# Kernel tuning notes

Measured on AMD Instinct MI355X. Metric: run time of the kernel, lower is better.

The kernel has to match this reference:

```python
import jax, jax.numpy as jnp
import numpy as np

N_HEAD = 16
D_HEAD = 64
D_LATENT = 32
BLOCK_SIZE = 2048


def rope_cache(dim, max_seq_len, theta=10000.0):
    inv_freq = 1.0 / (theta ** (jnp.arange(0, dim, 2, dtype=jnp.float32) / dim))
    t = jnp.arange(max_seq_len, dtype=jnp.float32)
    freqs = jnp.einsum('i,j->ij', t, inv_freq)        # [T, dim/2]
    emb = jnp.concatenate([freqs, freqs], axis=-1)    # [T, dim]
    return jnp.cos(emb), jnp.sin(emb)


def apply_rope(x, cos, sin):
    # x: [B, H, T, C]; interleaved-pair rotation as in the torch module
    B, H, T, C = x.shape
    c = cos[:T][None, None]
    s = sin[:T][None, None]
    x1 = x[..., 0::2]
    x2 = x[..., 1::2]
    rotated = jnp.stack((-x2, x1), axis=-1).reshape(B, H, T, C)
    return x * c + rotated * s


def setup_inputs() -> dict:
    key = jax.random.key(0)
    ks = jax.random.split(key, 7)
    sd = 0.02
    return {
        'x':   jax.random.normal(ks[0], (2, 2048, 1024), dtype=jnp.float32),
        'Wq':  jax.random.normal(ks[1], (1024, 1024), dtype=jnp.float32) * sd,
        'Wk':  jax.random.normal(ks[2], (512, 1024), dtype=jnp.float32) * sd,
        'Wv':  jax.random.normal(ks[3], (512, 1024), dtype=jnp.float32) * sd,
        'Wku': jax.random.normal(ks[4], (64, 32), dtype=jnp.float32) * sd,
        'Wvu': jax.random.normal(ks[5], (64, 32), dtype=jnp.float32) * sd,
        'Wc':  jax.random.normal(ks[6], (1024, 1024), dtype=jnp.float32) * sd,
    }


def reference(x, Wq, Wk, Wv, Wku, Wvu, Wc):
    B, T, C = x.shape
    H, Dh, Dl = N_HEAD, D_HEAD, D_LATENT

    # latent KV (compressed cache entries)
    k_lat = (x @ Wk.T).reshape(B, T, H, Dl)   # [B,T,H,Dl]
    v_lat = (x @ Wv.T).reshape(B, T, H, Dl)

    # q and up-projected k/v -> [B,H,T,Dh]
    q = (x @ Wq.T).reshape(B, T, H, Dh).transpose(0, 2, 1, 3)
    k = jnp.einsum('bthl,dl->bhtd', k_lat, Wku)
    v = jnp.einsum('bthl,dl->bhtd', v_lat, Wvu)

    cos, sin = rope_cache(Dh, BLOCK_SIZE)
    q = apply_rope(q, cos, sin)
    k = apply_rope(k, cos, sin)

    scale = 1.0 / jnp.sqrt(jnp.asarray(Dh, dtype=x.dtype))
    att = jnp.einsum('bhqd,bhkd->bhqk', q, k) * scale   # [B,H,T,T]
    causal = jnp.tril(jnp.ones((T, T), dtype=bool))
    att = jnp.where(causal[None, None], att, -jnp.inf)
    att = jax.nn.softmax(att, axis=-1)

    y = jnp.einsum('bhqk,bhkd->bhqd', att, v)           # [B,H,T,Dh]
    y = y.transpose(0, 2, 1, 3).reshape(B, T, C) @ Wc.T  # [B,T,C]
    return y, k_lat, v_lat
```

## Files before the change

### kernel.cpp

```cpp
#include <hip/hip_runtime.h>
#include <math.h>

#define NHEAD  16
#define DHEAD  64
#define DLAT   32
#define TSEQ   2048
#define NBATCH 2
#define CDIM   1024
#define MROWS  (NBATCH*TSEQ)

typedef __attribute__((ext_vector_type(8))) short bf16x8;
typedef __attribute__((ext_vector_type(4))) short bf16x4;
typedef __attribute__((ext_vector_type(4))) float f32x4;

#define AS1 __attribute__((address_space(1)))
#define AS3 __attribute__((address_space(3)))

__device__ __forceinline__ unsigned short f2bf(float f) {
    union { float f; unsigned u; } v; v.f = f;
    unsigned r = v.u + 0x7fff + ((v.u >> 16) & 1);
    return (unsigned short)(r >> 16);
}

__device__ __forceinline__ unsigned pk2(float lo, float hi) {
    return (unsigned)f2bf(lo) | ((unsigned)f2bf(hi) << 16);
}

__device__ __forceinline__ unsigned pack_trunc(float hi, float lo) {
    return __builtin_amdgcn_perm(__float_as_uint(hi), __float_as_uint(lo), 0x07060302u);
}

__device__ __forceinline__ void gld_lds16(const unsigned short* g, unsigned short* l) {
    __builtin_amdgcn_global_load_lds((const AS1 void*)g, (AS3 void*)l, 16, 0, 0);
}

__device__ __forceinline__ f32x4 mfma_16x16x16_bf16(bf16x4 a, bf16x4 b, f32x4 c) {
#if __has_builtin(__builtin_amdgcn_mfma_f32_16x16x16bf16_1k)
    return __builtin_amdgcn_mfma_f32_16x16x16bf16_1k(a, b, c, 0, 0, 0);
#else
    asm volatile("v_mfma_f32_16x16x16_bf16 %0, %1, %2, %0\n\ts_nop 4"
                 : "+v"(c) : "v"(a), "v"(b));
    return c;
#endif
}

#define QSCALE 0.18033688011112042f
#define RFREQ  0.28782313662425572f

__global__ __launch_bounds__(256) void cvt_all(
        const float* __restrict__ x,  const float* __restrict__ wq,
        const float* __restrict__ wk, const float* __restrict__ wv,
        const float* __restrict__ wc, const float* __restrict__ wku,
        const float* __restrict__ wvu,
        unsigned short* __restrict__ xb, unsigned short* __restrict__ wall) {
    int i = (blockIdx.x * 256 + threadIdx.x) * 4;
    const float* src; unsigned short* dst; int off;
    if      (i < 4194304) { src = x;   dst = xb;             off = 0;       }
    else if (i < 5242880) { src = wq;  dst = wall;           off = 4194304; }
    else if (i < 5767168) { src = wk;  dst = wall + 1048576; off = 5242880; }
    else if (i < 6291456) { src = wv;  dst = wall + 1572864; off = 5767168; }
    else if (i < 7340032) { src = wc;  dst = wall + 2097152; off = 6291456; }
    else if (i < 7342080) { src = wku; dst = wall + 3145728; off = 7340032; }
    else                  { src = wvu; dst = wall + 3147776; off = 7342080; }
    float4 v = *(const float4*)(src + (i - off));
    ushort4 o = { f2bf(v.x), f2bf(v.y), f2bf(v.z), f2bf(v.w) };
    *(ushort4*)(dst + (i - off)) = o;
}

__device__ __forceinline__ void gemm_core(
        const unsigned short* __restrict__ A, const unsigned short* __restrict__ W,
        int K, int bm, int bn, unsigned short* As, unsigned short* Bs,
        f32x4 (&acc)[2][2]) {
    const int tid = threadIdx.x;
    const int w = tid >> 6, lane = tid & 63;
    const int quad = lane >> 4, l16 = lane & 15;
    const int wm = (w >> 1) * 32, wn = (w & 1) * 32;

    const int r8 = lane >> 3, c8 = lane & 7;
    const int scl = (c8 ^ r8) * 8;

    const unsigned short* Ag0 = A + (size_t)(bm +      w*8 + r8) * K + scl;
    const unsigned short* Ag1 = A + (size_t)(bm + 64 + w*8 + r8) * K + scl;
    const unsigned short* Wg0 = W + (size_t)(bn +      w*8 + r8) * K + scl;
    unsigned short* AsD0 = &As[(     w*8) * 64];
    unsigned short* AsD1 = &As[(64 + w*8) * 64];
    unsigned short* BsD  = &Bs[(     w*8) * 64];

    const int fx0 = (quad ^ (l16 & 7)) * 8;
    const int fx1 = ((quad + 4) ^ (l16 & 7)) * 8;

    for (int k0 = 0; k0 < K; k0 += 64) {
        gld_lds16(Ag0 + k0, AsD0);
        gld_lds16(Ag1 + k0, AsD1);
        gld_lds16(Wg0 + k0, BsD);
        __syncthreads();
        bf16x8 af0[2], af1[2], bf0[2], bf1[2];
        #pragma unroll
        for (int t = 0; t < 2; ++t) {
            af0[t] = *(const bf16x8*)&As[(wm + t*16 + l16)*64 + fx0];
            af1[t] = *(const bf16x8*)&As[(wm + t*16 + l16)*64 + fx1];
        }
        #pragma unroll
        for (int c = 0; c < 2; ++c) {
            bf0[c] = *(const bf16x8*)&Bs[(wn + c*16 + l16)*64 + fx0];
            bf1[c] = *(const bf16x8*)&Bs[(wn + c*16 + l16)*64 + fx1];
        }
        #pragma unroll
        for (int t = 0; t < 2; ++t)
            #pragma unroll
            for (int c = 0; c < 2; ++c) {
                acc[t][c] = __builtin_amdgcn_mfma_f32_16x16x32_bf16(af0[t], bf0[c], acc[t][c], 0, 0, 0);
                acc[t][c] = __builtin_amdgcn_mfma_f32_16x16x32_bf16(af1[t], bf1[c], acc[t][c], 0, 0, 0);
            }
        __syncthreads();
    }
}

__global__ __launch_bounds__(512, 4) void gemm_proj(
        const unsigned short* __restrict__ A, const unsigned short* __restrict__ W,
        unsigned short* __restrict__ qbo, float* __restrict__ okl,
        float* __restrict__ ovl, int K) {
    __shared__ unsigned short As[128*64];
    __shared__ unsigned short Bs[64*64];
    const int bm = blockIdx.y * 128, bn = blockIdx.x * 64;
    f32x4 acc[2][2] = {};
    gemm_core(A, W, K, bm, bn, As, Bs, acc);

    const int tid = threadIdx.x;
    const int w = tid >> 6, lane = tid & 63;
    const int quad = lane >> 4, l16 = lane & 15;
    const int wm = (w >> 1) * 32, wn = (w & 1) * 32;

    if (bn < 1024) {
        const int h = bn >> 6;
        const int p = l16 & 1;
        const float invf0 = __expf(-(float)(l16)      * RFREQ);
        const float invf1 = __expf(-(float)(16 + l16) * RFREQ);
        #pragma unroll
        for (int t = 0; t < 2; ++t)
            #pragma unroll
            for (int r = 0; r < 4; ++r) {
                int row = bm + wm + t*16 + quad*4 + r;
                int ts  = row & 2047;
                float tf = (float)ts;
                size_t obase = (((size_t)((row >> 11)*16 + h))*TSEQ + ts)*DHEAD;
                #pragma unroll
                for (int c = 0; c < 2; ++c) {
                    float x  = acc[t][c][r];
                    float px = __shfl_xor(x, 1, 64);
                    float sv, cv;
                    __sincosf(tf * (c ? invf1 : invf0), &sv, &cv);
                    float o = (x*cv + (p ? px : -px)*sv) * QSCALE;
                    float po = __shfl_xor(o, 1, 64);
                    if (!p) {
                        unsigned pr = pk2(o, po);
                        *(unsigned*)&qbo[obase + wn + c*16 + l16] = pr;
                    }
                }
            }
    } else {
        float* base; int ldo;
        if (bn < 1536) { base = okl + (bn - 1024); ldo = 512; }
        else           { base = ovl + (bn - 1536); ldo = 512; }
        #pragma unroll
        for (int t = 0; t < 2; ++t)
            #pragma unroll
            for (int c = 0; c < 2; ++c)
                #pragma unroll
                for (int r = 0; r < 4; ++r) {
                    int row = bm + wm + t*16 + quad*4 + r;
                    int col = wn + c*16 + l16;
                    base[(size_t)row * ldo + col] = acc[t][c][r];
                }
    }
}

__global__ __launch_bounds__(512, 4) void gemm_out(
        const unsigned short* __restrict__ A, const unsigned short* __restrict__ W,
        float* __restrict__ O, int N, int K) {
    __shared__ unsigned short As[128*64];
    __shared__ unsigned short Bs[64*64];
    const int bm = blockIdx.y * 128, bn = blockIdx.x * 64;
    f32x4 acc[2][2] = {};
    gemm_core(A, W, K, bm, bn, As, Bs, acc);

    const int tid = threadIdx.x;
    const int w = tid >> 6, lane = tid & 63;
    const int quad = lane >> 4, l16 = lane & 15;
    const int wm = (w >> 1) * 32, wn = (w & 1) * 32;
    #pragma unroll
    for (int t = 0; t < 2; ++t)
        #pragma unroll
        for (int c = 0; c < 2; ++c)
            #pragma unroll
            for (int r = 0; r < 4; ++r) {
                int row = bm + wm + t*16 + quad*4 + r;
                int col = bn + wn + c*16 + l16;
                O[(size_t)row * N + col] = acc[t][c][r];
            }
}

__global__ __launch_bounds__(256) void latup(
        const float* __restrict__ klat, const float* __restrict__ vlat,
        const unsigned short* __restrict__ wkub, const unsigned short* __restrict__ wvub,
        unsigned short* __restrict__ kb, unsigned short* __restrict__ vt) {
    __shared__ __attribute__((aligned(16))) unsigned short ksh[4][16][72];
    __shared__ __attribute__((aligned(16))) unsigned short vsh[4][64][24];

    const int bh = blockIdx.y, b = bh >> 4, h = bh & 15;
    const int tid = threadIdx.x, w = tid >> 6, lane = tid & 63;
    const int quad = lane >> 4, l16 = lane & 15;
    const int tw = blockIdx.x * 64 + w * 16;
    const int t  = tw + l16;

    const float* klp = klat + ((size_t)(b*TSEQ + t))*(NHEAD*DLAT) + h*DLAT + quad*8;
    const float* vlp = vlat + ((size_t)(b*TSEQ + t))*(NHEAD*DLAT) + h*DLAT + quad*8;
    float4 kA = *(const float4*)klp, kB = *(const float4*)(klp + 4);
    float4 vA = *(const float4*)vlp, vB = *(const float4*)(vlp + 4);

    bf16x8 xk[4], xv[4];
    #pragma unroll
    for (int c = 0; c < 4; ++c) {
        xk[c] = *(const bf16x8*)&wkub[(c*16 + l16)*DLAT + quad*8];
        xv[c] = *(const bf16x8*)&wvub[(c*16 + l16)*DLAT + quad*8];
    }

    union { bf16x8 v; unsigned u[4]; } yk, yv;
    yk.u[0] = pk2(kA.x, kA.y); yk.u[1] = pk2(kA.z, kA.w);
    yk.u[2] = pk2(kB.x, kB.y); yk.u[3] = pk2(kB.z, kB.w);
    yv.u[0] = pk2(vA.x, vA.y); yv.u[1] = pk2(vA.z, vA.w);
    yv.u[2] = pk2(vB.x, vB.y); yv.u[3] = pk2(vB.z, vB.w);

    f32x4 aK[4], aV[4];
    #pragma unroll
    for (int c = 0; c < 4; ++c) {
        f32x4 z = {0.f, 0.f, 0.f, 0.f};
        aK[c] = __builtin_amdgcn_mfma_f32_16x16x32_bf16(xk[c], yk.v, z, 0, 0, 0);
        aV[c] = __builtin_amdgcn_mfma_f32_16x16x32_bf16(xv[c], yv.v, z, 0, 0, 0);
    }

    float C0[4], S0[4], C1[4], S1[4];
    const float tf = (float)t;
    #pragma unroll
    for (int j = 0; j < 4; ++j) {
        float f0 = (float)(quad*4 + j);
        __sincosf(tf * __expf(-f0 * RFREQ),          &S0[j], &C0[j]);
        __sincosf(tf * __expf(-(f0 + 16.f) * RFREQ), &S1[j], &C1[j]);
    }

    #pragma unroll
    for (int c = 0; c < 4; ++c) {
        const float* Cs = (c & 1) ? C1 : C0;
        const float* Ss = (c & 1) ? S1 : S0;
        float a0 = aK[c][0], a1 = aK[c][1], a2 = aK[c][2], a3 = aK[c][3];
        unsigned kw0 = pk2(a0*Cs[0] - a1*Ss[0], a1*Cs[1] + a0*Ss[1]);
        unsigned kw1 = pk2(a2*Cs[2] - a3*Ss[2], a3*Cs[3] + a2*Ss[3]);
        *(uint2*)&ksh[w][l16][c*16 + quad*4] = make_uint2(kw0, kw1);

        vsh[w][c*16 + quad*4 + 0][l16] = f2bf(aV[c][0]);
        vsh[w][c*16 + quad*4 + 1][l16] = f2bf(aV[c][1]);
        vsh[w][c*16 + quad*4 + 2][l16] = f2bf(aV[c][2]);
        vsh[w][c*16 + quad*4 + 3][l16] = f2bf(aV[c][3]);
    }

    __asm__ __volatile__("s_waitcnt lgkmcnt(0)" ::: "memory");

    const int ro = lane >> 2, co = (lane & 3) * 16;
    size_t go = ((size_t)bh*TSEQ + tw + ro)*DHEAD + co;
    int4 k0o = *(const int4*)&ksh[w][ro][co];
    int4 k1o = *(const int4*)&ksh[w][ro][co + 8];
    *(int4*)&kb[go]     = k0o;
    *(int4*)&kb[go + 8] = k1o;

    size_t vo = ((size_t)bh*DHEAD + lane)*TSEQ + tw;
    int4 v0o = *(const int4*)&vsh[w][lane][0];
    int4 v1o = *(const int4*)&vsh[w][lane][8];
    *(int4*)&vt[vo]     = v0o;
    *(int4*)&vt[vo + 8] = v1o;
}

__device__ __forceinline__ void online_sm(f32x4 (&s)[8], float& m_run, float& l_run,
                                          f32x4 (&o)[4]) {
    float mx = -1e30f;
    #pragma unroll
    for (int c = 0; c < 8; ++c)
        #pragma unroll
        for (int r = 0; r < 4; ++r) mx = fmaxf(mx, s[c][r]);
    mx = fmaxf(mx, __shfl_xor(mx, 16, 64));
    mx = fmaxf(mx, __shfl_xor(mx, 32, 64));
    if (!__all(mx <= m_run + 8.f)) {
        float mn = fmaxf(m_run, mx);
        float alpha = __builtin_exp2f(m_run - mn);
        m_run = mn;
        l_run *= alpha;
        #pragma unroll
        for (int c = 0; c < 4; ++c)
            #pragma unroll
            for (int r = 0; r < 4; ++r) o[c][r] *= alpha;
    }
    float ls = 0.f;
    #pragma unroll
    for (int c = 0; c < 8; ++c)
        #pragma unroll
        for (int r = 0; r < 4; ++r) {
            float p = __builtin_exp2f(s[c][r] - m_run);
            s[c][r] = p;
            ls += p;
        }
    ls += __shfl_xor(ls, 16, 64);
    ls += __shfl_xor(ls, 32, 64);
    l_run += ls;
}

__global__ __launch_bounds__(512, 4) void flash_attn(
        const unsigned short* __restrict__ qb, const unsigned short* __restrict__ kb,
        const unsigned short* __restrict__ vtb, unsigned short* __restrict__ yatt) {
    const int bh = blockIdx.x;
    const int b = bh >> 4, h = bh & 15;

    __shared__ unsigned short Ks[2][128][64];
    __shared__ unsigned short VTs[2][64][128];

    const int tid  = threadIdx.x;
    const int w    = tid >> 6;
    const int lane = tid & 63;
    const int quad = lane >> 4;
    const int l16  = lane & 15;
    const bool heavy = (w >= 4);
    const int wq = w & 3;

    const int qtA = blockIdx.y;
    const int qtB = 31 - qtA;
    const int qt  = heavy ? qtB : qtA;
    const int myN = (qt + 2) >> 1;
    const int nB  = (qtB + 2) >> 1;

    const unsigned short* Kbase = kb  + (size_t)bh * TSEQ * DHEAD;
    const unsigned short* Vbase = vtb + (size_t)bh * DHEAD * TSEQ;

    const int kr8 = lane >> 3, kc8 = lane & 7;
    const int kcl = (kc8 ^ kr8) * 8;
    const int vr4 = lane >> 4, vcp = lane & 15;

    const int kx0 = (quad ^ (l16 & 7)) * 8;
    const int kx1 = ((quad + 4) ^ (l16 & 7)) * 8;
    const int vq = (quad >> 1), vodd = (quad & 1) * 4;

    const unsigned short* qbase =
        qb + ((size_t)bh*TSEQ + qt*64 + wq*16 + l16) * DHEAD + quad*8;
    bf16x8 q0 = *(const bf16x8*)qbase;
    bf16x8 q1 = *(const bf16x8*)(qbase + 32);

    f32x4 oacc[4] = {};
    float m_run = -1e30f, l_run = 0.f;

    #pragma unroll
    for (int i = 0; i < 2; ++i) {
        gld_lds16(Kbase + (size_t)(w*16 + i*8 + kr8)*DHEAD + kcl,
                  &Ks[0][w*16 + i*8][0]);
        int vrow = w*8 + i*4 + vr4;
        int vcl = (vcp ^ (vrow & 15)) * 8;
        gld_lds16(Vbase + (size_t)vrow*TSEQ + vcl, &VTs[0][w*8 + i*4][0]);
    }
    __syncthreads();

    for (int j = 0; j < nB; ++j) {
        const int buf = j & 1;
        if (j + 1 < nB) {
            const int kc = (j + 1) * 128;
            #pragma unroll
            for (int i = 0; i < 2; ++i) {
                gld_lds16(Kbase + (size_t)(kc + w*16 + i*8 + kr8)*DHEAD + kcl,
                          &Ks[buf^1][w*16 + i*8][0]);
                int vrow = w*8 + i*4 + vr4;
                int vcl = (vcp ^ (vrow & 15)) * 8;
                gld_lds16(Vbase + (size_t)vrow*TSEQ + kc + vcl,
                          &VTs[buf^1][w*8 + i*4][0]);
            }
        }

        if (j < myN) {
            f32x4 s[8];
            __builtin_amdgcn_s_setprio(1);
            #pragma unroll
            for (int c = 0; c < 8; ++c) {
                bf16x8 ak0 = *(const bf16x8*)&Ks[buf][c*16 + l16][kx0];
                bf16x8 ak1 = *(const bf16x8*)&Ks[buf][c*16 + l16][kx1];
                f32x4 z = {0.f, 0.f, 0.f, 0.f};
                z = __builtin_amdgcn_mfma_f32_16x16x32_bf16(ak0, q0, z, 0, 0, 0);
                z = __builtin_amdgcn_mfma_f32_16x16x32_bf16(ak1, q1, z, 0, 0, 0);
                s[c] = z;
            }
            __builtin_amdgcn_s_setprio(0);

            if (j == myN - 1) {
                #pragma unroll
                for (int c = 0; c < 8; ++c)
                    #pragma unroll
                    for (int r = 0; r < 4; ++r)
                        if (j*128 + c*16 + quad*4 + r > qt*64 + wq*16 + l16)
                            s[c][r] = -1e30f;
            }

            online_sm(s, m_run, l_run, oacc);

            __builtin_amdgcn_s_setprio(1);
            #pragma unroll
            for (int c = 0; c < 8; ++c) {
                union { bf16x4 v; unsigned u[2]; } bP;
                bP.u[0] = pack_trunc(s[c][1], s[c][0]);
                bP.u[1] = pack_trunc(s[c][3], s[c][2]);
                const int vcol = ((2*c + vq) ^ l16) * 8 + vodd;
                #pragma unroll
                for (int dc = 0; dc < 4; ++dc) {
                    bf16x4 av = *(const bf16x4*)&VTs[buf][dc*16 + l16][vcol];
                    oacc[dc] = mfma_16x16x16_bf16(av, bP.v, oacc[dc]);
                }
            }
            __builtin_amdgcn_s_setprio(0);
        }

        __syncthreads();
    }

    float invl = 1.0f / l_run;
    unsigned short* Wt = &Ks[0][0][0] + w * (16*72);
    #pragma unroll
    for (int c = 0; c < 4; ++c)
        #pragma unroll
        for (int r = 0; r < 4; ++r)
            Wt[(size_t)l16*72 + c*16 + quad*4 + r] = f2bf(oacc[c][r] * invl);
    __asm__ __volatile__("" ::: "memory");
    #pragma unroll
    for (int p = 0; p < 2; ++p) {
        int row = p*8 + (lane >> 3);
        int d0 = (lane & 7) * 8;
        int4 val = *(const int4*)&Wt[row*72 + d0];
        int tg = qt*64 + wq*16 + row;
        *(int4*)&yatt[((size_t)(b*TSEQ + tg))*CDIM + h*DHEAD + d0] = val;
    }
}

extern "C" void kernel_launch(void* const* d_in, const int* in_sizes, int n_in,
                              void* d_out, int out_size, void* d_ws, size_t ws_size,
                              hipStream_t stream) {
    const float* x   = (const float*)d_in[0];
    const float* Wq  = (const float*)d_in[1];
    const float* Wk  = (const float*)d_in[2];
    const float* Wv  = (const float*)d_in[3];
    const float* Wku = (const float*)d_in[4];
    const float* Wvu = (const float*)d_in[5];
    const float* Wc  = (const float*)d_in[6];

    float* out_y  = (float*)d_out;
    float* out_kl = out_y  + (size_t)MROWS * CDIM;
    float* out_vl = out_kl + (size_t)MROWS * NHEAD*DLAT;

    float* qproj = (float*)d_ws;
    unsigned short* xb   = (unsigned short*)(qproj + (size_t)MROWS*CDIM);
    unsigned short* qb   = xb  + (size_t)MROWS*CDIM;
    unsigned short* kb   = qb  + (size_t)MROWS*CDIM;
    unsigned short* vt   = kb  + (size_t)MROWS*CDIM;
    unsigned short* wall = vt  + (size_t)MROWS*CDIM;
    unsigned short* wcb  = wall + (size_t)2048*CDIM;
    unsigned short* wkub = wall + 3145728;
    unsigned short* wvub = wall + 3147776;
    unsigned short* yatt = (unsigned short*)qproj;

    cvt_all<<<7172, 256, 0, stream>>>(x, Wq, Wk, Wv, Wc, Wku, Wvu, xb, wall);

    gemm_proj<<<dim3(2048/64, MROWS/128), 512, 0, stream>>>(
        xb, wall, qb, out_kl, out_vl, CDIM);

    latup<<<dim3(TSEQ/64, NBATCH*NHEAD), 256, 0, stream>>>(
        out_kl, out_vl, wkub, wvub, kb, vt);

    flash_attn<<<dim3(NBATCH*NHEAD, 16), 512, 0, stream>>>(qb, kb, vt, yatt);

    gemm_out<<<dim3(CDIM/64, MROWS/128), 512, 0, stream>>>(yatt, wcb, out_y, CDIM, CDIM);
}
```

Measured before the change: 188.4 us.

## Double-buffer LDS tiles in projection GEMMs to overlap loads with MFMA

The shared GEMM core now keeps two LDS buffers per operand and prefetches the next K-tile into the idle buffer while MFMAs run on the current one. This drops one of the two barriers per K iteration and hides global-to-LDS latency behind compute. LDS use per block doubles to 48 KB, and launch bounds go from 4 to 6 blocks, which tightens the register budget and may limit occupancy. Only the projection and output GEMMs are affected; the attention kernel is unchanged.

```diff
diff --git a/kernel.cpp b/kernel.cpp
--- a/kernel.cpp
+++ b/kernel.cpp
@@ -89,39 +89,51 @@
     const int fx0 = (quad ^ (l16 & 7)) * 8;
     const int fx1 = ((quad + 4) ^ (l16 & 7)) * 8;
 
-    for (int k0 = 0; k0 < K; k0 += 64) {
-        gld_lds16(Ag0 + k0, AsD0);
-        gld_lds16(Ag1 + k0, AsD1);
-        gld_lds16(Wg0 + k0, BsD);
+    const int nt = K >> 6;
+
+    gld_lds16(Ag0, AsD0);
+    gld_lds16(Ag1, AsD1);
+    gld_lds16(Wg0, BsD);
+    __syncthreads();
+
+    for (int t = 0; t < nt; ++t) {
+        const int buf = t & 1;
+        if (t + 1 < nt) {
+            const int k0 = (t + 1) * 64;
+            gld_lds16(Ag0 + k0, AsD0 + (buf^1)*8192);
+            gld_lds16(Ag1 + k0, AsD1 + (buf^1)*8192);
+            gld_lds16(Wg0 + k0, BsD  + (buf^1)*4096);
+        }
+        const unsigned short* Ab = As + buf*8192;
+        const unsigned short* Bb = Bs + buf*4096;
+        bf16x8 af0[2], af1[2], bf0[2], bf1[2];
+        #pragma unroll
+        for (int t2 = 0; t2 < 2; ++t2) {
+            af0[t2] = *(const bf16x8*)&Ab[(wm + t2*16 + l16)*64 + fx0];
+            af1[t2] = *(const bf16x8*)&Ab[(wm + t2*16 + l16)*64 + fx1];
+        }
+        #pragma unroll
+        for (int c = 0; c < 2; ++c) {
+            bf0[c] = *(const bf16x8*)&Bb[(wn + c*16 + l16)*64 + fx0];
+            bf1[c] = *(const bf16x8*)&Bb[(wn + c*16 + l16)*64 + fx1];
+        }
+        #pragma unroll
+        for (int t2 = 0; t2 < 2; ++t2)
+            #pragma unroll
+            for (int c = 0; c < 2; ++c) {
+                acc[t2][c] = __builtin_amdgcn_mfma_f32_16x16x32_bf16(af0[t2], bf0[c], acc[t2][c], 0, 0, 0);
+                acc[t2][c] = __builtin_amdgcn_mfma_f32_16x16x32_bf16(af1[t2], bf1[c], acc[t2][c], 0, 0, 0);
+            }
         __syncthreads();
-        bf16x8 af0[2], af1[2], bf0[2], bf1[2];
-        #pragma unroll
-        for (int t = 0; t < 2; ++t) {
-            af0[t] = *(const bf16x8*)&As[(wm + t*16 + l16)*64 + fx0];
-            af1[t] = *(const bf16x8*)&As[(wm + t*16 + l16)*64 + fx1];
-        }
-        #pragma unroll
-        for (int c = 0; c < 2; ++c) {
-            bf0[c] = *(const bf16x8*)&Bs[(wn + c*16 + l16)*64 + fx0];
-            bf1[c] = *(const bf16x8*)&Bs[(wn + c*16 + l16)*64 + fx1];
-        }
-        #pragma unroll
-        for (int t = 0; t < 2; ++t)
-            #pragma unroll
-            for (int c = 0; c < 2; ++c) {
-                acc[t][c] = __builtin_amdgcn_mfma_f32_16x16x32_bf16(af0[t], bf0[c], acc[t][c], 0, 0, 0);
-                acc[t][c] = __builtin_amdgcn_mfma_f32_16x16x32_bf16(af1[t], bf1[c], acc[t][c], 0, 0, 0);
-            }
-        __syncthreads();
-    }
-}
-
-__global__ __launch_bounds__(512, 4) void gemm_proj(
+    }
+}
+
+__global__ __launch_bounds__(512, 6) void gemm_proj(
         const unsigned short* __restrict__ A, const unsigned short* __restrict__ W,
         unsigned short* __restrict__ qbo, float* __restrict__ okl,
         float* __restrict__ ovl, int K) {
-    __shared__ unsigned short As[128*64];
-    __shared__ unsigned short Bs[64*64];
+    __shared__ unsigned short As[2*128*64];
+    __shared__ unsigned short Bs[2*64*64];
     const int bm = blockIdx.y * 128, bn = blockIdx.x * 64;
     f32x4 acc[2][2] = {};
     gemm_core(A, W, K, bm, bn, As, Bs, acc);
@@ -175,11 +187,11 @@
     }
 }
 
-__global__ __launch_bounds__(512, 4) void gemm_out(
+__global__ __launch_bounds__(512, 6) void gemm_out(
         const unsigned short* __restrict__ A, const unsigned short* __restrict__ W,
         float* __restrict__ O, int N, int K) {
-    __shared__ unsigned short As[128*64];
-    __shared__ unsigned short Bs[64*64];
+    __shared__ unsigned short As[2*128*64];
+    __shared__ unsigned short Bs[2*64*64];
     const int bm = blockIdx.y * 128, bn = blockIdx.x * 64;
     f32x4 acc[2][2] = {};
     gemm_core(A, W, K, bm, bn, As, Bs, acc);
```

Measured after the change: 182.2 us. 3.3% less time.
